# Kernel tuning notes

Hardware: AMD Instinct MI355X
Metric: run time of the kernel (lower is better)

The kernel has to match this reference:

```python
import jax, jax.numpy as jnp
import numpy as np

DIM = 512
NUM_HEADS = 8
HEAD_DIM = DIM // NUM_HEADS


def setup_inputs() -> dict:
    key = jax.random.key(0)
    ks = jax.random.split(key, 9)
    s = 1.0 / np.sqrt(DIM)
    x = jax.random.normal(ks[0], (2, 4096, DIM), dtype=jnp.float32)
    Wq = jax.random.uniform(ks[1], (DIM, DIM), jnp.float32, -s, s)
    bq = jax.random.uniform(ks[2], (DIM,), jnp.float32, -s, s)
    Wk = jax.random.uniform(ks[3], (DIM, DIM), jnp.float32, -s, s)
    bk = jax.random.uniform(ks[4], (DIM,), jnp.float32, -s, s)
    Wv = jax.random.uniform(ks[5], (DIM, DIM), jnp.float32, -s, s)
    bv = jax.random.uniform(ks[6], (DIM,), jnp.float32, -s, s)
    Wo = jax.random.uniform(ks[7], (DIM, DIM), jnp.float32, -s, s)
    bo = jax.random.uniform(ks[8], (DIM,), jnp.float32, -s, s)
    return {"x": x, "Wq": Wq, "bq": bq, "Wk": Wk, "bk": bk,
            "Wv": Wv, "bv": bv, "Wo": Wo, "bo": bo}


def reference(x, Wq, bq, Wk, bk, Wv, bv, Wo, bo):
    B, S, D = x.shape
    H, Hd = NUM_HEADS, HEAD_DIM
    # Linear layers (torch stores weight as [out,in]; here W is [in,out])
    q = (x @ Wq + bq).reshape(B, S, H, Hd).transpose(0, 2, 1, 3)  # [B,H,S,Hd]
    k = (x @ Wk + bk).reshape(B, S, H, Hd).transpose(0, 2, 1, 3)
    v = (x @ Wv + bv).reshape(B, S, H, Hd).transpose(0, 2, 1, 3)
    # NOTE: original scales by dim**0.5, not head_dim**0.5
    energy = jnp.einsum('bhqd,bhkd->bhqk', q, k) / jnp.sqrt(jnp.float32(D))
    attn = jax.nn.softmax(energy, axis=-1)
    out = jnp.einsum('bhqk,bhkd->bhqd', attn, v)
    out = out.transpose(0, 2, 1, 3).reshape(B, S, D)
    return out @ Wo + bo
```

## Files before the change

### kernel.cpp

```cpp
#include <hip/hip_runtime.h>

typedef unsigned short USH;
typedef short s16x8 __attribute__((ext_vector_type(8)));
typedef float f32x4 __attribute__((ext_vector_type(4)));
typedef float f32x4v __attribute__((ext_vector_type(4)));
typedef unsigned int u32x4 __attribute__((ext_vector_type(4)));
typedef s16x8 s16x8_a __attribute__((may_alias));
typedef f32x4v f32x4v_a __attribute__((may_alias));
typedef u32x4 u32x4_a __attribute__((may_alias));
typedef unsigned long long u64_a __attribute__((may_alias));

#if __has_builtin(__builtin_amdgcn_exp2f)
#define EXP2F(x) __builtin_amdgcn_exp2f(x)
#else
#define EXP2F(x) __builtin_exp2f(x)
#endif

__device__ __forceinline__ USH f2bf(float f) {
  union { float f; unsigned int i; } c; c.f = f;
  unsigned int x = c.i;
  return (USH)((x + 0x7FFFu + ((x >> 16) & 1u)) >> 16);
}
__device__ __forceinline__ unsigned int pk_bf16(float a, float b) {
#if __has_builtin(__builtin_amdgcn_cvt_pk_bf16_f32)
  typedef USH ush2 __attribute__((ext_vector_type(2)));
  union { ush2 v; unsigned int u; } r;
  r.v = __builtin_amdgcn_cvt_pk_bf16_f32(a, b);
  return r.u;
#else
  union { float f; unsigned int i; } ca, cb; ca.f = a; cb.f = b;
  return ((ca.i + 0x8000u) >> 16) | ((cb.i + 0x8000u) & 0xFFFF0000u);
#endif
}

__device__ __forceinline__ f32x4 mfma16(s16x8 a, s16x8 b, f32x4 c) {
  return __builtin_amdgcn_mfma_f32_16x16x32_bf16(a, b, c, 0, 0, 0);
}

#if __has_builtin(__builtin_amdgcn_global_load_lds)
__device__ __forceinline__ void gld_lds16(const USH* g, USH* l) {
  __builtin_amdgcn_global_load_lds(
      static_cast<const unsigned int __attribute__((address_space(1)))*>(
          (const void __attribute__((address_space(1)))*)g),
      static_cast<unsigned int __attribute__((address_space(3)))*>(
          (void __attribute__((address_space(3)))*)l),
      16, 0, 0);
}
#else
__device__ __forceinline__ void gld_lds16(const USH* g, USH* l) {
  *(s16x8_a*)l = *(const s16x8_a*)g;
}
#endif

__global__ __launch_bounds__(256) void prep(
    const float* __restrict__ Wq, const float* __restrict__ Wk,
    const float* __restrict__ Wv, const float* __restrict__ Wo,
    const float* __restrict__ x, USH* __restrict__ wsT, USH* __restrict__ xb) {
  __shared__ float tile[32][33];
  const int z = blockIdx.z;
  const int t = threadIdx.x;
  if (z == 4) {
    const size_t b0 = ((size_t)blockIdx.y * 16 + blockIdx.x) * 16384;
    #pragma unroll
    for (int j = 0; j < 8; ++j) {
      const size_t i = b0 + (size_t)j * 2048 + t * 8;
      const f32x4v a = *(const f32x4v_a*)(x + i);
      const f32x4v b = *(const f32x4v_a*)(x + i + 4);
      u32x4 s;
      s.x = pk_bf16(a.x, a.y); s.y = pk_bf16(a.z, a.w);
      s.z = pk_bf16(b.x, b.y); s.w = pk_bf16(b.z, b.w);
      *(u32x4_a*)(xb + i) = s;
    }
    return;
  }
  const float* W = (z == 0) ? Wq : (z == 1) ? Wk : (z == 2) ? Wv : Wo;
  USH* WT = wsT + (size_t)z * 262144;
  const int n0 = blockIdx.x * 32, k0 = blockIdx.y * 32;
  const int tx = t & 31, ty = t >> 5;
  #pragma unroll
  for (int i = 0; i < 4; ++i)
    tile[ty + i * 8][tx] = W[(size_t)(k0 + ty + i * 8) * 512 + n0 + tx];
  __syncthreads();
  #pragma unroll
  for (int i = 0; i < 4; ++i)
    WT[(size_t)(n0 + ty + i * 8) * 512 + k0 + tx] = f2bf(tile[tx][ty + i * 8]);
}

template <int MODE>
__global__ __launch_bounds__(256, 3) void gemm_bias(
    const USH* __restrict__ A, const USH* __restrict__ BT0,
    const float* __restrict__ b0, const float* __restrict__ b1,
    const float* __restrict__ b2,
    USH* __restrict__ oQ, USH* __restrict__ oKV, float* __restrict__ oF) {
  __shared__ __align__(16) USH As[128 * 68];
  __shared__ __align__(16) USH Bs[128 * 68];
  const int z = blockIdx.z;
  const USH* BT = BT0 + (size_t)z * 262144;
  const float* bias = (z == 0) ? b0 : ((z == 1) ? b1 : b2);
  USH* outb = (z == 0) ? oQ : (oKV + (size_t)(z - 1) * 4194304);
  const float qs = (MODE == 1 && z == 0) ? 0.06375871528132839f : 1.0f;

  const int t = threadIdx.x;
  const int w = t >> 6, lane = t & 63;
  const int c = lane & 15, g = lane >> 4;
  const int wm = w & 1, wn = w >> 1;
  const int m0 = blockIdx.x * 128, n0 = blockIdx.y * 128;
  const int srow = t >> 1, scol = (t & 1) * 32;

  f32x4 acc[4][4] = {};

  const USH* Ap0 = A + (size_t)(m0 + srow) * 512 + scol;
  const USH* Bp0 = BT + (size_t)(n0 + srow) * 512 + scol;
  s16x8 pa[4], pb[4];
  #pragma unroll
  for (int j = 0; j < 4; ++j) {
    pa[j] = *(const s16x8_a*)(Ap0 + j * 8);
    pb[j] = *(const s16x8_a*)(Bp0 + j * 8);
  }

  for (int kt = 0; kt < 8; ++kt) {
    __syncthreads();
    #pragma unroll
    for (int j = 0; j < 4; ++j) {
      *(s16x8_a*)(As + srow * 68 + scol + j * 8) = pa[j];
      *(s16x8_a*)(Bs + srow * 68 + scol + j * 8) = pb[j];
    }
    const int ktn = (kt < 7) ? kt + 1 : kt;
    #pragma unroll
    for (int j = 0; j < 4; ++j) {
      pa[j] = *(const s16x8_a*)(Ap0 + ktn * 64 + j * 8);
      pb[j] = *(const s16x8_a*)(Bp0 + ktn * 64 + j * 8);
    }
    __syncthreads();
    #pragma unroll
    for (int ks = 0; ks < 2; ++ks) {
      s16x8 af[4], bfr[4];
      #pragma unroll
      for (int i = 0; i < 4; ++i) {
        af[i]  = *(const s16x8_a*)(As + (wm * 64 + i * 16 + c) * 68 + ks * 32 + g * 8);
        bfr[i] = *(const s16x8_a*)(Bs + (wn * 64 + i * 16 + c) * 68 + ks * 32 + g * 8);
      }
      #pragma unroll
      for (int mf = 0; mf < 4; ++mf)
        #pragma unroll
        for (int nf = 0; nf < 4; ++nf)
          acc[mf][nf] = mfma16(af[mf], bfr[nf], acc[mf][nf]);
    }
  }

  #pragma unroll
  for (int nf = 0; nf < 4; ++nf) {
    const int n = n0 + wn * 64 + nf * 16 + c;
    const float bv = bias[n];
    #pragma unroll
    for (int mf = 0; mf < 4; ++mf)
      #pragma unroll
      for (int r = 0; r < 4; ++r) {
        const int m = m0 + wm * 64 + mf * 16 + g * 4 + r;
        const float v = (acc[mf][nf][r] + bv) * qs;
        if (MODE == 0) {
          oF[(size_t)m * 512 + n] = v;
        } else {
          const int bb = m >> 12, s = m & 4095, h = n >> 6, hd = n & 63;
          if (z == 2)
            outb[(((size_t)(bb * 8 + h)) * 64 + hd) * 4096 + s] = f2bf(v);
          else
            outb[(((size_t)(bb * 8 + h)) * 4096 + s) * 64 + hd] = f2bf(v);
        }
      }
  }
}

__global__ __launch_bounds__(512, 4) void attn(const USH* __restrict__ Qbuf,
                                               const USH* __restrict__ kv,
                                               USH* __restrict__ att) {
  __shared__ __align__(16) USH Ks[2 * 4096];
  __shared__ __align__(16) USH Vt[2 * 4096];
  __shared__ __align__(16) USH Ps[8][16 * 76];
  __shared__ float lbuf[8][16];

  const int t = threadIdx.x;
  const int w = t >> 6, lane = t & 63;
  const int c = lane & 15, g = lane >> 4;
  const int linear = blockIdx.x + (blockIdx.y << 5);
  const int xcd = linear & 7, idx = linear >> 3;
  const int bh = xcd + ((idx >> 5) << 3);
  const int bb = bh >> 3, hh = bh & 7;
  const size_t base = (size_t)bh * 262144;
  const USH* Q = Qbuf + base;
  const USH* K = kv + base;
  const USH* V = kv + 4194304 + base;
  const int q0 = (idx & 31) * 128 + w * 16;

  s16x8 qf[2];
  #pragma unroll
  for (int kh = 0; kh < 2; ++kh)
    qf[kh] = *(const s16x8_a*)(Q + (size_t)(q0 + c) * 64 + kh * 32 + g * 8);

  s16x8 onesf;
  {
    const short one = (short)0x3F80, val = (c == 0) ? one : (short)0;
    #pragma unroll
    for (int j = 0; j < 8; ++j) onesf[j] = val;
  }

  f32x4 o[4] = {};
  f32x4 o_l = {};

  const int pK = w * 16 + (lane >> 2);
  const int keyK = pK & 63, halfK = pK >> 6;
  const int ccK = (lane & 3) ^ ((keyK >> 1) & 3);
  const USH* gK0 = K + (size_t)keyK * 64 + halfK * 32 + ccK * 8;
  const int hdV = w * 8 + (lane >> 3);
  const int ccV = (lane & 7) ^ (hdV & 7);
  const USH* gV0 = V + (size_t)hdV * 4096 + ccV * 8;
  USH* lK = Ks + w * 512 + lane * 8;
  USH* lV = Vt + w * 512 + lane * 8;

  gld_lds16(gK0, lK);
  gld_lds16(gV0, lV);

  for (int kt = 0; kt < 64; ++kt) {
    const int buf = kt & 1;
    __syncthreads();
    if (kt < 63) {
      const int nb = (buf ^ 1) * 4096;
      gld_lds16(gK0 + (size_t)(kt + 1) * 4096, lK + nb);
      gld_lds16(gV0 + (size_t)(kt + 1) * 64, lV + nb);
    }

    f32x4 st[4] = {};
    #pragma unroll
    for (int kh = 0; kh < 2; ++kh) {
      s16x8 ak[4];
      #pragma unroll
      for (int kff = 0; kff < 4; ++kff) {
        const int row = kff * 16 + c;
        const int qsw = (g ^ ((c >> 1) & 3)) * 8;
        ak[kff] = *(const s16x8_a*)(Ks + buf * 4096 + kh * 2048 + row * 32 + qsw);
      }
      #pragma unroll
      for (int kff = 0; kff < 4; ++kff)
        st[kff] = mfma16(ak[kff], qf[kh], st[kff]);
    }

    #pragma unroll
    for (int kff = 0; kff < 4; ++kff)
      #pragma unroll
      for (int r = 0; r < 4; ++r)
        st[kff][r] = EXP2F(st[kff][r]);

    #pragma unroll
    for (int kff = 0; kff < 4; ++kff) {
      const unsigned int lo = pk_bf16(st[kff][0], st[kff][1]);
      const unsigned int hi = pk_bf16(st[kff][2], st[kff][3]);
      *(u64_a*)(&Ps[w][c * 76 + kff * 16 + g * 4]) =
          (unsigned long long)lo | ((unsigned long long)hi << 32);
    }

    #pragma unroll
    for (int kf = 0; kf < 2; ++kf) {
      const s16x8 ap = *(const s16x8_a*)(&Ps[w][c * 76 + kf * 32 + g * 8]);
      s16x8 bv[4];
      #pragma unroll
      for (int hf = 0; hf < 4; ++hf) {
        const int qv = ((kf * 4 + g) ^ (c & 7)) * 8;
        bv[hf] = *(const s16x8_a*)(Vt + buf * 4096 + (c + 16 * hf) * 64 + qv);
      }
      #pragma unroll
      for (int hf = 0; hf < 4; ++hf)
        o[hf] = mfma16(ap, bv[hf], o[hf]);
      o_l = mfma16(ap, onesf, o_l);
    }
  }

  if (c == 0) {
    #pragma unroll
    for (int r = 0; r < 4; ++r) lbuf[w][g * 4 + r] = o_l[r];
  }
  __syncthreads();

  #pragma unroll
  for (int r = 0; r < 4; ++r) {
    const int ml = g * 4 + r;
    const float linv = 1.0f / lbuf[w][ml];
    const int qrow = q0 + ml;
    #pragma unroll
    for (int hf = 0; hf < 4; ++hf) {
      const int hd = c + 16 * hf;
      att[((size_t)(bb * 4096 + qrow)) * 512 + hh * 64 + hd] =
          f2bf(o[hf][r] * linv);
    }
  }
}

extern "C" void kernel_launch(void* const* d_in, const int* in_sizes, int n_in,
                              void* d_out, int out_size, void* d_ws, size_t ws_size,
                              hipStream_t stream) {
  (void)in_sizes; (void)n_in; (void)out_size; (void)ws_size;
  const float* x  = (const float*)d_in[0];
  const float* Wq = (const float*)d_in[1];
  const float* bq = (const float*)d_in[2];
  const float* Wk = (const float*)d_in[3];
  const float* bk = (const float*)d_in[4];
  const float* Wv = (const float*)d_in[5];
  const float* bv = (const float*)d_in[6];
  const float* Wo = (const float*)d_in[7];
  const float* bo = (const float*)d_in[8];
  USH* ws  = (USH*)d_ws;
  USH* wT  = ws;
  USH* kv  = ws + 1048576;
  USH* att = ws + 1048576 + 8388608;
  float* outF = (float*)d_out;
  USH* qscratch = (USH*)d_out;
  USH* xb = (USH*)d_out + 4194304;

  prep<<<dim3(16, 16, 5), 256, 0, stream>>>(Wq, Wk, Wv, Wo, x, wT, xb);
  gemm_bias<1><<<dim3(64, 4, 3), 256, 0, stream>>>(xb, wT, bq, bk, bv,
                                                   qscratch, kv, nullptr);
  attn<<<dim3(32, 16), 512, 0, stream>>>(qscratch, kv, att);
  gemm_bias<0><<<dim3(64, 4, 1), 256, 0, stream>>>(att, wT + 3 * 262144, bo, bo, bo,
                                                   nullptr, nullptr, outF);
}
```

Baseline: 208.0 us.

## Process two query tiles per wave in attention to reuse K/V fragments

The attention kernel drops from 8 waves to 4 waves per block, and each wave now handles 32 query rows instead of 16. K and V fragments read from LDS are reused across both query sub-tiles, which halves LDS reads per MFMA. Each thread now issues two global-to-LDS loads per tile to keep the same K/V tile size. The cost is more accumulator registers per wave and fewer waves available to hide latency.

Result: no change. 210.0 us (+1.0%).

```diff
diff --git a/kernel.cpp b/kernel.cpp
--- a/kernel.cpp
+++ b/kernel.cpp
@@ -171,13 +171,13 @@
   }
 }
 
-__global__ __launch_bounds__(512, 4) void attn(const USH* __restrict__ Qbuf,
+__global__ __launch_bounds__(256, 2) void attn(const USH* __restrict__ Qbuf,
                                                const USH* __restrict__ kv,
                                                USH* __restrict__ att) {
   __shared__ __align__(16) USH Ks[2 * 4096];
   __shared__ __align__(16) USH Vt[2 * 4096];
-  __shared__ __align__(16) USH Ps[8][16 * 76];
-  __shared__ float lbuf[8][16];
+  __shared__ __align__(16) USH Ps[4][32 * 76];
+  __shared__ float lbuf[4][32];
 
   const int t = threadIdx.x;
   const int w = t >> 6, lane = t & 63;
@@ -190,12 +190,14 @@
   const USH* Q = Qbuf + base;
   const USH* K = kv + base;
   const USH* V = kv + 4194304 + base;
-  const int q0 = (idx & 31) * 128 + w * 16;
-
-  s16x8 qf[2];
-  #pragma unroll
-  for (int kh = 0; kh < 2; ++kh)
-    qf[kh] = *(const s16x8_a*)(Q + (size_t)(q0 + c) * 64 + kh * 32 + g * 8);
+  const int q0 = (idx & 31) * 128 + w * 32;
+
+  s16x8 qf[2][2];
+  #pragma unroll
+  for (int qi = 0; qi < 2; ++qi)
+    #pragma unroll
+    for (int kh = 0; kh < 2; ++kh)
+      qf[qi][kh] = *(const s16x8_a*)(Q + (size_t)(q0 + qi * 16 + c) * 64 + kh * 32 + g * 8);
 
   s16x8 onesf;
   {
@@ -204,32 +206,37 @@
     for (int j = 0; j < 8; ++j) onesf[j] = val;
   }
 
-  f32x4 o[4] = {};
-  f32x4 o_l = {};
-
-  const int pK = w * 16 + (lane >> 2);
-  const int keyK = pK & 63, halfK = pK >> 6;
+  f32x4 o[2][4] = {};
+  f32x4 o_l[2] = {};
+
+  const int keyK = w * 16 + (lane >> 2);
   const int ccK = (lane & 3) ^ ((keyK >> 1) & 3);
-  const USH* gK0 = K + (size_t)keyK * 64 + halfK * 32 + ccK * 8;
+  const USH* gK0 = K + (size_t)keyK * 64 + ccK * 8;
   const int hdV = w * 8 + (lane >> 3);
   const int ccV = (lane & 7) ^ (hdV & 7);
   const USH* gV0 = V + (size_t)hdV * 4096 + ccV * 8;
   USH* lK = Ks + w * 512 + lane * 8;
   USH* lV = Vt + w * 512 + lane * 8;
 
-  gld_lds16(gK0, lK);
-  gld_lds16(gV0, lV);
+  #pragma unroll
+  for (int j = 0; j < 2; ++j) {
+    gld_lds16(gK0 + j * 32, lK + j * 2048);
+    gld_lds16(gV0 + (size_t)j * 131072, lV + j * 2048);
+  }
 
   for (int kt = 0; kt < 64; ++kt) {
     const int buf = kt & 1;
     __syncthreads();
     if (kt < 63) {
       const int nb = (buf ^ 1) * 4096;
-      gld_lds16(gK0 + (size_t)(kt + 1) * 4096, lK + nb);
-      gld_lds16(gV0 + (size_t)(kt + 1) * 64, lV + nb);
-    }
-
-    f32x4 st[4] = {};
+      #pragma unroll
+      for (int j = 0; j < 2; ++j) {
+        gld_lds16(gK0 + (size_t)(kt + 1) * 4096 + j * 32, lK + nb + j * 2048);
+        gld_lds16(gV0 + (size_t)(kt + 1) * 64 + (size_t)j * 131072, lV + nb + j * 2048);
+      }
+    }
+
+    f32x4 st[2][4] = {};
     #pragma unroll
     for (int kh = 0; kh < 2; ++kh) {
       s16x8 ak[4];
@@ -240,27 +247,36 @@
         ak[kff] = *(const s16x8_a*)(Ks + buf * 4096 + kh * 2048 + row * 32 + qsw);
       }
       #pragma unroll
+      for (int qi = 0; qi < 2; ++qi)
+        #pragma unroll
+        for (int kff = 0; kff < 4; ++kff)
+          st[qi][kff] = mfma16(ak[kff], qf[qi][kh], st[qi][kff]);
+    }
+
+    #pragma unroll
+    for (int qi = 0; qi < 2; ++qi)
+      #pragma unroll
       for (int kff = 0; kff < 4; ++kff)
-        st[kff] = mfma16(ak[kff], qf[kh], st[kff]);
-    }
-
-    #pragma unroll
-    for (int kff = 0; kff < 4; ++kff)
-      #pragma unroll
-      for (int r = 0; r < 4; ++r)
-        st[kff][r] = EXP2F(st[kff][r]);
-
-    #pragma unroll
-    for (int kff = 0; kff < 4; ++kff) {
-      const unsigned int lo = pk_bf16(st[kff][0], st[kff][1]);
-      const unsigned int hi = pk_bf16(st[kff][2], st[kff][3]);
-      *(u64_a*)(&Ps[w][c * 76 + kff * 16 + g * 4]) =
-          (unsigned long long)lo | ((unsigned long long)hi << 32);
-    }
+        #pragma unroll
+        for (int r = 0; r < 4; ++r)
+          st[qi][kff][r] = EXP2F(st[qi][kff][r]);
+
+    #pragma unroll
+    for (int qi = 0; qi < 2; ++qi)
+      #pragma unroll
+      for (int kff = 0; kff < 4; ++kff) {
+        const unsigned int lo = pk_bf16(st[qi][kff][0], st[qi][kff][1]);
+        const unsigned int hi = pk_bf16(st[qi][kff][2], st[qi][kff][3]);
+        *(u64_a*)(&Ps[w][(qi * 16 + c) * 76 + kff * 16 + g * 4]) =
+            (unsigned long long)lo | ((unsigned long long)hi << 32);
+      }
 
     #pragma unroll
     for (int kf = 0; kf < 2; ++kf) {
-      const s16x8 ap = *(const s16x8_a*)(&Ps[w][c * 76 + kf * 32 + g * 8]);
+      s16x8 ap[2];
+      #pragma unroll
+      for (int qi = 0; qi < 2; ++qi)
+        ap[qi] = *(const s16x8_a*)(&Ps[w][(qi * 16 + c) * 76 + kf * 32 + g * 8]);
       s16x8 bv[4];
       #pragma unroll
       for (int hf = 0; hf < 4; ++hf) {
@@ -268,30 +284,37 @@
         bv[hf] = *(const s16x8_a*)(Vt + buf * 4096 + (c + 16 * hf) * 64 + qv);
       }
       #pragma unroll
-      for (int hf = 0; hf < 4; ++hf)
-        o[hf] = mfma16(ap, bv[hf], o[hf]);
-      o_l = mfma16(ap, onesf, o_l);
+      for (int qi = 0; qi < 2; ++qi) {
+        #pragma unroll
+        for (int hf = 0; hf < 4; ++hf)
+          o[qi][hf] = mfma16(ap[qi], bv[hf], o[qi][hf]);
+        o_l[qi] = mfma16(ap[qi], onesf, o_l[qi]);
+      }
     }
   }
 
   if (c == 0) {
     #pragma unroll
-    for (int r = 0; r < 4; ++r) lbuf[w][g * 4 + r] = o_l[r];
+    for (int qi = 0; qi < 2; ++qi)
+      #pragma unroll
+      for (int r = 0; r < 4; ++r) lbuf[w][qi * 16 + g * 4 + r] = o_l[qi][r];
   }
   __syncthreads();
 
   #pragma unroll
-  for (int r = 0; r < 4; ++r) {
-    const int ml = g * 4 + r;
-    const float linv = 1.0f / lbuf[w][ml];
-    const int qrow = q0 + ml;
-    #pragma unroll
-    for (int hf = 0; hf < 4; ++hf) {
-      const int hd = c + 16 * hf;
-      att[((size_t)(bb * 4096 + qrow)) * 512 + hh * 64 + hd] =
-          f2bf(o[hf][r] * linv);
-    }
-  }
+  for (int qi = 0; qi < 2; ++qi)
+    #pragma unroll
+    for (int r = 0; r < 4; ++r) {
+      const int ml = qi * 16 + g * 4 + r;
+      const float linv = 1.0f / lbuf[w][ml];
+      const int qrow = q0 + ml;
+      #pragma unroll
+      for (int hf = 0; hf < 4; ++hf) {
+        const int hd = c + 16 * hf;
+        att[((size_t)(bb * 4096 + qrow)) * 512 + hh * 64 + hd] =
+            f2bf(o[qi][hf][r] * linv);
+      }
+    }
 }
 
 extern "C" void kernel_launch(void* const* d_in, const int* in_sizes, int n_in,
@@ -318,7 +341,7 @@
   prep<<<dim3(16, 16, 5), 256, 0, stream>>>(Wq, Wk, Wv, Wo, x, wT, xb);
   gemm_bias<1><<<dim3(64, 4, 3), 256, 0, stream>>>(xb, wT, bq, bk, bv,
                                                    qscratch, kv, nullptr);
-  attn<<<dim3(32, 16), 512, 0, stream>>>(qscratch, kv, att);
+  attn<<<dim3(32, 16), 256, 0, stream>>>(qscratch, kv, att);
   gemm_bias<0><<<dim3(64, 4, 1), 256, 0, stream>>>(att, wT + 3 * 262144, bo, bo, bo,
                                                    nullptr, nullptr, outF);
 }
```
